# Kernel tuning notes

Hardware: AMD Instinct MI355X
Metric: run time of the kernel (lower is better)

The kernel has to match this reference:

```python
import jax, jax.numpy as jnp
import numpy as np

B, T, C, H = 2, 2048, 1024, 16
HS = C // H  # head_size = 64
EPS = 1e-5


def _layernorm(x, w, b):
    mu = jnp.mean(x, axis=-1, keepdims=True)
    var = jnp.mean(jnp.square(x - mu), axis=-1, keepdims=True)
    return (x - mu) * jax.lax.rsqrt(var + EPS) * w + b


def setup_inputs() -> dict:
    key = jax.random.key(0)
    ks = jax.random.split(key, 12)
    s_attn = 1.0 / np.sqrt(C)
    s_ff1 = 1.0 / np.sqrt(C)
    s_ff2 = 1.0 / np.sqrt(4 * C)
    return {
        "x": jax.random.normal(ks[0], (B, T, C), dtype=jnp.float32),
        "ln1_w": jnp.ones((C,), jnp.float32),
        "ln1_b": jnp.zeros((C,), jnp.float32),
        "Wq": jax.random.normal(ks[1], (H, C, HS), jnp.float32) * s_attn,
        "Wk": jax.random.normal(ks[2], (H, C, HS), jnp.float32) * s_attn,
        "Wv": jax.random.normal(ks[3], (H, C, HS), jnp.float32) * s_attn,
        "proj_w": jax.random.normal(ks[4], (C, C), jnp.float32) * s_attn,
        "proj_b": jnp.zeros((C,), jnp.float32),
        "ln2_w": jnp.ones((C,), jnp.float32),
        "ln2_b": jnp.zeros((C,), jnp.float32),
        "fc1_w": jax.random.normal(ks[5], (C, 4 * C), jnp.float32) * s_ff1,
        "fc1_b": jnp.zeros((4 * C,), jnp.float32),
        "fc2_w": jax.random.normal(ks[6], (4 * C, C), jnp.float32) * s_ff2,
        "fc2_b": jnp.zeros((C,), jnp.float32),
    }


def reference(x, ln1_w, ln1_b, Wq, Wk, Wv, proj_w, proj_b, ln2_w, ln2_b, fc1_w, fc1_b, fc2_w, fc2_b):
    Bx, Tx, Cx = x.shape
    # --- self-attention with pre-norm residual ---
    h = _layernorm(x, ln1_w, ln1_b)                       # [B,T,C]
    q = jnp.einsum("btc,hcd->bhtd", h, Wq)                 # [B,H,T,HS]
    k = jnp.einsum("btc,hcd->bhtd", h, Wk)
    v = jnp.einsum("btc,hcd->bhtd", h, Wv)
    # NOTE: original code applies NO 1/sqrt(d) scaling -- keep faithful.
    wei = jnp.einsum("bhtd,bhsd->bhts", q, k)              # [B,H,T,T]
    causal = jnp.tril(jnp.ones((Tx, Tx), dtype=bool))
    wei = jnp.where(causal, wei, -jnp.inf)
    wei = jax.nn.softmax(wei, axis=-1)
    attn = jnp.einsum("bhts,bhsd->bhtd", wei, v)           # [B,H,T,HS]
    attn = attn.transpose(0, 2, 1, 3).reshape(Bx, Tx, Cx)  # concat heads
    sa = attn @ proj_w + proj_b                            # output projection
    x = x + sa
    # --- FFN with pre-norm residual ---
    h2 = _layernorm(x, ln2_w, ln2_b)
    ff = jax.nn.relu(h2 @ fc1_w + fc1_b) @ fc2_w + fc2_b
    return x + ff
```

## Files before the change

kernel.cpp:

```cpp
#include <hip/hip_runtime.h>
#include <hip/hip_bf16.h>

#define Bn 2
#define Tn 2048
#define Cn 1024
#define Hn 16
#define HSn 64
#define Mn (Bn*Tn)
#define LN_EPS 1e-5f

typedef unsigned short u16;
typedef __attribute__((ext_vector_type(8))) short bf16x8;
typedef __attribute__((ext_vector_type(4))) float f32x4;

#define MFMA16(a,b,c) __builtin_amdgcn_mfma_f32_16x16x32_bf16(a, b, c, 0, 0, 0)
#define GLL16(g,l) __builtin_amdgcn_global_load_lds( \
    (const __attribute__((address_space(1))) void*)(g), \
    (__attribute__((address_space(3))) void*)(l), 16, 0, 0)

__device__ __forceinline__ u16 f2b(float f) {
    unsigned int u = __float_as_uint(f);
    unsigned int r = (u + 0x7FFFu + ((u >> 16) & 1u)) >> 16;
    return (u16)r;
}
__device__ __forceinline__ float b2f(unsigned u) {
    return __uint_as_float(u << 16);
}
__device__ __forceinline__ unsigned cvtpk(float lo, float hi) {
    unsigned r;
    asm("v_cvt_pk_bf16_f32 %0, %1, %2" : "=v"(r) : "v"(lo), "v"(hi));
    return r;
}

__global__ __launch_bounds__(256) void wqkv_t(
    const float* __restrict__ Wq, const float* __restrict__ Wk,
    const float* __restrict__ Wv, u16* __restrict__ Wt)
{
    int z = blockIdx.z, h = blockIdx.y, c0 = blockIdx.x * 64;
    const float* in = (z == 0 ? Wq : z == 1 ? Wk : Wv) + (size_t)h * 65536;
    __shared__ float t[64][68];
    int tid = threadIdx.x;
#pragma unroll
    for (int it = 0; it < 4; it++) {
        int r = it * 16 + (tid >> 4);
        *(float4*)&t[r][(tid & 15) * 4] =
            *(const float4*)(in + (size_t)(c0 + r) * 64 + (tid & 15) * 4);
    }
    __syncthreads();
    int d = tid >> 2, seg = tid & 3;
    union { u16 u[8]; uint4 q; } pk;
#pragma unroll
    for (int hq = 0; hq < 2; hq++) {
#pragma unroll
        for (int j = 0; j < 8; j++) pk.u[j] = f2b(t[seg * 16 + hq * 8 + j][d]);
        *(uint4*)(Wt + (size_t)(z * 1024 + h * 64 + d) * 1024 + c0 + seg * 16 + hq * 8) = pk.q;
    }
}

__global__ __launch_bounds__(256) void transpose_cvt(
    const float* __restrict__ in, u16* __restrict__ out, int R, int C)
{
    __shared__ float t[64][68];
    int r0 = blockIdx.y * 64, c0 = blockIdx.x * 64;
    int tid = threadIdx.x;
#pragma unroll
    for (int it = 0; it < 4; it++) {
        int r = it * 16 + (tid >> 4);
        *(float4*)&t[r][(tid & 15) * 4] =
            *(const float4*)(in + (size_t)(r0 + r) * C + c0 + (tid & 15) * 4);
    }
    __syncthreads();
    int c = tid >> 2, seg = tid & 3;
    union { u16 u[8]; uint4 q; } pk;
#pragma unroll
    for (int hq = 0; hq < 2; hq++) {
#pragma unroll
        for (int j = 0; j < 8; j++) pk.u[j] = f2b(t[seg * 16 + hq * 8 + j][c]);
        *(uint4*)(out + (size_t)(c0 + c) * R + r0 + seg * 16 + hq * 8) = pk.q;
    }
}

__global__ __launch_bounds__(256) void ln_bf16(
    const float* __restrict__ x, const float* __restrict__ w,
    const float* __restrict__ bvec, u16* __restrict__ out)
{
    int row  = blockIdx.x * 4 + (threadIdx.x >> 6);
    int lane = threadIdx.x & 63;
    const float* xr = x + (size_t)row * Cn;
    float4 v[4];
    float s = 0.f, sq = 0.f;
#pragma unroll
    for (int i = 0; i < 4; i++) {
        v[i] = *(const float4*)(xr + lane * 4 + i * 256);
        s  += v[i].x + v[i].y + v[i].z + v[i].w;
        sq += v[i].x * v[i].x + v[i].y * v[i].y + v[i].z * v[i].z + v[i].w * v[i].w;
    }
#pragma unroll
    for (int off = 1; off < 64; off <<= 1) {
        s  += __shfl_xor(s, off);
        sq += __shfl_xor(sq, off);
    }
    float mu   = s * (1.f / Cn);
    float var  = sq * (1.f / Cn) - mu * mu;
    float rstd = rsqrtf(var + LN_EPS);
    u16* orow = out + (size_t)row * Cn;
#pragma unroll
    for (int i = 0; i < 4; i++) {
        float4 w4 = *(const float4*)(w    + lane * 4 + i * 256);
        float4 b4 = *(const float4*)(bvec + lane * 4 + i * 256);
        union { u16 u[4]; uint2 q; } pk;
        pk.u[0] = f2b((v[i].x - mu) * rstd * w4.x + b4.x);
        pk.u[1] = f2b((v[i].y - mu) * rstd * w4.y + b4.y);
        pk.u[2] = f2b((v[i].z - mu) * rstd * w4.z + b4.z);
        pk.u[3] = f2b((v[i].w - mu) * rstd * w4.w + b4.w);
        *(uint2*)(orow + lane * 4 + i * 256) = pk.q;
    }
}

template<int OBF, int BIAS, int RELU>
__global__ __launch_bounds__(512, 2) void gemm_8ph(
    const u16* __restrict__ A, const u16* __restrict__ Bt,
    const float* __restrict__ bias, void* Cout,
    int M, int N, int K, int NT)
{
    __shared__ u16 lds[65536];
    const int tid = threadIdx.x, l = tid & 63, w = tid >> 6;
    const int wm = w >> 2, wn = w & 3;
    const int g = l >> 4, c16 = l & 15;

    const int nwg = (int)gridDim.x, cpx = nwg >> 3;
    const int bid = (int)blockIdx.x;
    const int sbid = (bid & 7) * cpx + (bid >> 3);
    const int m0 = (sbid / NT) * 256, n0 = (sbid % NT) * 256;

    const int sr = tid >> 3;
    const int ss = ((tid & 7) ^ (sr & 7)) << 3;
    const u16* Asrc = A  + (size_t)(m0 + sr) * K + ss;
    const u16* Bsrc = Bt + (size_t)(n0 + sr) * K + ss;
    const int dst0 = tid * 8;

#define ST_A8(d_, h_, kt_) do {                                              \
        GLL16(Asrc + (size_t)((h_) * 128) * K + (size_t)(kt_) * 64,          \
              &lds[(d_) * 32768 + (h_) * 8192 + dst0]);                      \
        GLL16(Asrc + (size_t)((h_) * 128 + 64) * K + (size_t)(kt_) * 64,     \
              &lds[(d_) * 32768 + (h_) * 8192 + 4096 + dst0]);               \
    } while (0)
#define ST_B8(d_, h_, kt_) do {                                              \
        GLL16(Bsrc + (size_t)((h_) * 128) * K + (size_t)(kt_) * 64,          \
              &lds[(d_) * 32768 + 16384 + (h_) * 8192 + dst0]);              \
        GLL16(Bsrc + (size_t)((h_) * 128 + 64) * K + (size_t)(kt_) * 64,     \
              &lds[(d_) * 32768 + 16384 + (h_) * 8192 + 4096 + dst0]);       \
    } while (0)
#define LDA8(d_, mi_, s_) (*(const bf16x8*)&lds[(d_) * 32768 +               \
        (wm * 128 + (mi_) * 16 + c16) * 64 +                                  \
        ((((s_) * 4 + g) ^ ((wm * 128 + (mi_) * 16 + c16) & 7)) << 3)])
#define LDB8(d_, nj_, s_) (*(const bf16x8*)&lds[(d_) * 32768 + 16384 +       \
        (wn * 64 + (nj_) * 16 + c16) * 64 +                                   \
        ((((s_) * 4 + g) ^ ((wn * 64 + (nj_) * 16 + c16) & 7)) << 3)])
#define PH_HEAD() do {                                                       \
        __builtin_amdgcn_s_barrier();                                        \
        asm volatile("s_waitcnt lgkmcnt(0)" ::: "memory");                   \
        __builtin_amdgcn_sched_barrier(0);                                   \
        __builtin_amdgcn_s_setprio(1);                                       \
    } while (0)
#define PH_MFMA(NH_) do {                                                    \
        _Pragma("unroll")                                                    \
        for (int mi = 0; mi < 8; mi++) {                                     \
            acc[mi][2*(NH_)]   = MFMA16(aF[mi], bF[0], acc[mi][2*(NH_)]);    \
            acc[mi][2*(NH_)+1] = MFMA16(aF[mi], bF[1], acc[mi][2*(NH_)+1]);  \
        }                                                                    \
    } while (0)

    f32x4 acc[8][4];
#pragma unroll
    for (int i = 0; i < 8; i++)
#pragma unroll
        for (int j = 0; j < 4; j++) acc[i][j] = (f32x4){0.f, 0.f, 0.f, 0.f};

    const int nk = K >> 6;
    ST_A8(0, 0, 0); ST_A8(0, 1, 0); ST_B8(0, 0, 0); ST_B8(0, 1, 0);
    ST_A8(1, 0, 1); ST_A8(1, 1, 1);
    asm volatile("s_waitcnt vmcnt(4)" ::: "memory");
    __builtin_amdgcn_s_barrier();

    bf16x8 aF[8], bF[2];
    for (int m = 0; m < nk; m++) {
        const int d = m & 1, dn = d ^ 1;
#pragma unroll
        for (int mi = 0; mi < 8; mi++) aF[mi] = LDA8(d, mi, 0);
        bF[0] = LDB8(d, 0, 0); bF[1] = LDB8(d, 1, 0);
        if (m + 1 < nk) ST_B8(dn, 0, m + 1);
        PH_HEAD(); PH_MFMA(0);
        __builtin_amdgcn_s_setprio(0);
        __builtin_amdgcn_s_barrier();
        bF[0] = LDB8(d, 2, 0); bF[1] = LDB8(d, 3, 0);
        if (m + 1 < nk) ST_B8(dn, 1, m + 1);
        PH_HEAD(); PH_MFMA(1);
        __builtin_amdgcn_s_setprio(0);
        __builtin_amdgcn_s_barrier();
#pragma unroll
        for (int mi = 0; mi < 8; mi++) aF[mi] = LDA8(d, mi, 1);
        bF[0] = LDB8(d, 0, 1); bF[1] = LDB8(d, 1, 1);
        PH_HEAD(); PH_MFMA(0);
        __builtin_amdgcn_s_setprio(0);
        __builtin_amdgcn_s_barrier();
        bF[0] = LDB8(d, 2, 1); bF[1] = LDB8(d, 3, 1);
        if (m + 2 < nk) { ST_A8(d, 0, m + 2); ST_A8(d, 1, m + 2); }
        PH_HEAD(); PH_MFMA(1);
        __builtin_amdgcn_s_setprio(0);
        if (m + 1 < nk) {
            if (m + 2 < nk) asm volatile("s_waitcnt vmcnt(4)" ::: "memory");
            else            asm volatile("s_waitcnt vmcnt(0)" ::: "memory");
        }
        __builtin_amdgcn_s_barrier();
    }
#undef ST_A8
#undef ST_B8
#undef LDA8
#undef LDB8
#undef PH_HEAD
#undef PH_MFMA

#pragma unroll
    for (int mi = 0; mi < 8; mi++)
#pragma unroll
        for (int nj = 0; nj < 4; nj++) {
            const int coln = n0 + wn * 64 + nj * 16 + c16;
            float bv = BIAS ? bias[coln] : 0.f;
#pragma unroll
            for (int reg = 0; reg < 4; reg++) {
                int rowm = m0 + wm * 128 + mi * 16 + 4 * g + reg;
                float v = acc[mi][nj][reg] + bv;
                if (RELU) v = fmaxf(v, 0.f);
                if (OBF) ((u16*)Cout)[(size_t)rowm * N + coln] = f2b(v);
                else     ((float*)Cout)[(size_t)rowm * N + coln] = v;
            }
        }
}

__global__ __launch_bounds__(512, 1) void gemm_qkv(
    const u16* __restrict__ A, const u16* __restrict__ Bt,
    u16* __restrict__ Cout)
{
    __shared__ u16 lds[57344];
    const int tid = threadIdx.x, l = tid & 63, w = tid >> 6;
    const int wm = w >> 1, wn = w & 1;
    const int g = l >> 4, c16 = l & 15;
    const int K = 1024, N = 3072;

    const int bid = (int)blockIdx.x;
    const int sbid = (bid & 7) * 32 + (bid >> 3);
    const int m0 = (sbid >> 4) * 256, n0 = (sbid & 15) * 192;

    const int sr = tid >> 3;
    const int ss = ((tid & 7) ^ (sr & 7)) << 3;
    const u16* Asrc = A  + (size_t)(m0 + sr) * K + ss;
    const u16* Bsrc = Bt + (size_t)(n0 + sr) * K + ss;
    const int dst0 = tid * 8;

#define ST_A(d_, h_, kt_) do {                                               \
        GLL16(Asrc + (size_t)((h_) * 128) * K + (size_t)(kt_) * 64,          \
              &lds[(d_) * 16384 + (h_) * 8192 + dst0]);                      \
        GLL16(Asrc + (size_t)((h_) * 128 + 64) * K + (size_t)(kt_) * 64,     \
              &lds[(d_) * 16384 + (h_) * 8192 + 4096 + dst0]);               \
    } while (0)
#define ST_B1(d_, seg_, kt_)                                                 \
        GLL16(Bsrc + (size_t)((seg_) * 64) * K + (size_t)(kt_) * 64,         \
              &lds[32768 + (d_) * 12288 + (seg_) * 4096 + dst0])
#define LDA(d_, mi_, s_) (*(const bf16x8*)&lds[(d_) * 16384 +                \
        (wm * 64 + (mi_) * 16 + c16) * 64 +                                   \
        ((((s_) * 4 + g) ^ ((wm * 64 + (mi_) * 16 + c16) & 7)) << 3)])
#define LDB(d_, nj_, s_) (*(const bf16x8*)&lds[32768 + (d_) * 12288 +        \
        (wn * 96 + (nj_) * 16 + c16) * 64 +                                   \
        ((((s_) * 4 + g) ^ ((wn * 96 + (nj_) * 16 + c16) & 7)) << 3)])
#define PH_HEAD() do {                                                       \
        __builtin_amdgcn_s_barrier();                                        \
        asm volatile("s_waitcnt lgkmcnt(0)" ::: "memory");                   \
        __builtin_amdgcn_sched_barrier(0);                                   \
        __builtin_amdgcn_s_setprio(1);                                       \
    } while (0)
#define PH_MFMA(NH_) do {                                                    \
        _Pragma("unroll")                                                    \
        for (int mi = 0; mi < 4; mi++) {                                     \
            acc[mi][3*(NH_)]   = MFMA16(aF[mi], bF[0], acc[mi][3*(NH_)]);    \
            acc[mi][3*(NH_)+1] = MFMA16(aF[mi], bF[1], acc[mi][3*(NH_)+1]);  \
            acc[mi][3*(NH_)+2] = MFMA16(aF[mi], bF[2], acc[mi][3*(NH_)+2]);  \
        }                                                                    \
    } while (0)

    f32x4 acc[4][6];
#pragma unroll
    for (int i = 0; i < 4; i++)
#pragma unroll
        for (int j = 0; j < 6; j++) acc[i][j] = (f32x4){0.f, 0.f, 0.f, 0.f};

    const int nk = 16;
    ST_A(0, 0, 0); ST_A(0, 1, 0);
    ST_B1(0, 0, 0); ST_B1(0, 1, 0); ST_B1(0, 2, 0);
    ST_A(1, 0, 1); ST_A(1, 1, 1);
    asm volatile("s_waitcnt vmcnt(4)" ::: "memory");
    __builtin_amdgcn_s_barrier();

    bf16x8 aF[4], bF[3];
    for (int m = 0; m < nk; m++) {
        const int d = m & 1, dn = d ^ 1;
#pragma unroll
        for (int mi = 0; mi < 4; mi++) aF[mi] = LDA(d, mi, 0);
        bF[0] = LDB(d, 0, 0); bF[1] = LDB(d, 1, 0); bF[2] = LDB(d, 2, 0);
        if (m + 1 < nk) { ST_B1(dn, 0, m + 1); ST_B1(dn, 1, m + 1); }
        PH_HEAD(); PH_MFMA(0);
        __builtin_amdgcn_s_setprio(0);
        __builtin_amdgcn_s_barrier();
        bF[0] = LDB(d, 3, 0); bF[1] = LDB(d, 4, 0); bF[2] = LDB(d, 5, 0);
        if (m + 1 < nk) ST_B1(dn, 2, m + 1);
        PH_HEAD(); PH_MFMA(1);
        __builtin_amdgcn_s_setprio(0);
        __builtin_amdgcn_s_barrier();
#pragma unroll
        for (int mi = 0; mi < 4; mi++) aF[mi] = LDA(d, mi, 1);
        bF[0] = LDB(d, 0, 1); bF[1] = LDB(d, 1, 1); bF[2] = LDB(d, 2, 1);
        PH_HEAD(); PH_MFMA(0);
        __builtin_amdgcn_s_setprio(0);
        __builtin_amdgcn_s_barrier();
        bF[0] = LDB(d, 3, 1); bF[1] = LDB(d, 4, 1); bF[2] = LDB(d, 5, 1);
        if (m + 2 < nk) { ST_A(d, 0, m + 2); ST_A(d, 1, m + 2); }
        PH_HEAD(); PH_MFMA(1);
        __builtin_amdgcn_s_setprio(0);
        if (m + 1 < nk) {
            if (m + 2 < nk) asm volatile("s_waitcnt vmcnt(4)" ::: "memory");
            else            asm volatile("s_waitcnt vmcnt(0)" ::: "memory");
        }
        __builtin_amdgcn_s_barrier();
    }
#undef ST_A
#undef ST_B1
#undef LDA
#undef LDB
#undef PH_HEAD
#undef PH_MFMA

#pragma unroll
    for (int mi = 0; mi < 4; mi++)
#pragma unroll
        for (int nj = 0; nj < 6; nj++) {
            const int coln = n0 + wn * 96 + nj * 16 + c16;
#pragma unroll
            for (int reg = 0; reg < 4; reg++) {
                int rowm = m0 + wm * 64 + mi * 16 + 4 * g + reg;
                Cout[(size_t)rowm * N + coln] = f2b(acc[mi][nj][reg]);
            }
        }
}

__global__ __launch_bounds__(512, 2) void gemm_fc2(
    const u16* __restrict__ A, const u16* __restrict__ Bt,
    u16* __restrict__ part)
{
    __shared__ u16 lds[65536];
    const int tid = threadIdx.x, l = tid & 63, w = tid >> 6;
    const int wm = w >> 2, wn = w & 3;
    const int g = l >> 4, c16 = l & 15;

    const int bid = (int)blockIdx.x;
    const int sbid = (bid & 7) * 32 + (bid >> 3);
    const int chunk = sbid >> 6, t = sbid & 63;
    const int m0 = (t >> 2) * 256, n0 = (t & 3) * 256;
    const int kB = chunk << 10;

    const int sr = tid >> 3;
    const int ss = ((tid & 7) ^ (sr & 7)) << 3;
    const u16* Asrc = A  + (size_t)(m0 + sr) * 4096 + kB + ss;
    const u16* Bsrc = Bt + (size_t)(n0 + sr) * 4096 + kB + ss;
    const int dst0 = tid * 8;

#define ST_A8(d_, h_, kt_) do {                                              \
        GLL16(Asrc + (size_t)((h_) * 128) * 4096 + (size_t)(kt_) * 64,       \
              &lds[(d_) * 32768 + (h_) * 8192 + dst0]);                      \
        GLL16(Asrc + (size_t)((h_) * 128 + 64) * 4096 + (size_t)(kt_) * 64,  \
              &lds[(d_) * 32768 + (h_) * 8192 + 4096 + dst0]);               \
    } while (0)
#define ST_B8(d_, h_, kt_) do {                                              \
        GLL16(Bsrc + (size_t)((h_) * 128) * 4096 + (size_t)(kt_) * 64,       \
              &lds[(d_) * 32768 + 16384 + (h_) * 8192 + dst0]);              \
        GLL16(Bsrc + (size_t)((h_) * 128 + 64) * 4096 + (size_t)(kt_) * 64,  \
              &lds[(d_) * 32768 + 16384 + (h_) * 8192 + 4096 + dst0]);       \
    } while (0)
#define LDA8(d_, mi_, s_) (*(const bf16x8*)&lds[(d_) * 32768 +               \
        (wm * 128 + (mi_) * 16 + c16) * 64 +                                  \
        ((((s_) * 4 + g) ^ ((wm * 128 + (mi_) * 16 + c16) & 7)) << 3)])
#define LDB8(d_, nj_, s_) (*(const bf16x8*)&lds[(d_) * 32768 + 16384 +       \
        (wn * 64 + (nj_) * 16 + c16) * 64 +                                   \
        ((((s_) * 4 + g) ^ ((wn * 64 + (nj_) * 16 + c16) & 7)) << 3)])
#define PH_HEAD() do {                                                       \
        __builtin_amdgcn_s_barrier();                                        \
        asm volatile("s_waitcnt lgkmcnt(0)" ::: "memory");                   \
        __builtin_amdgcn_sched_barrier(0);                                   \
        __builtin_amdgcn_s_setprio(1);                                       \
    } while (0)
#define PH_MFMA(NH_) do {                                                    \
        _Pragma("unroll")                                                    \
        for (int mi = 0; mi < 8; mi++) {                                     \
            acc[mi][2*(NH_)]   = MFMA16(aF[mi], bF[0], acc[mi][2*(NH_)]);    \
            acc[mi][2*(NH_)+1] = MFMA16(aF[mi], bF[1], acc[mi][2*(NH_)+1]);  \
        }                                                                    \
    } while (0)

    f32x4 acc[8][4];
#pragma unroll
    for (int i = 0; i < 8; i++)
#pragma unroll
        for (int j = 0; j < 4; j++) acc[i][j] = (f32x4){0.f, 0.f, 0.f, 0.f};

    const int nk = 16;
    ST_A8(0, 0, 0); ST_A8(0, 1, 0); ST_B8(0, 0, 0); ST_B8(0, 1, 0);
    ST_A8(1, 0, 1); ST_A8(1, 1, 1);
    asm volatile("s_waitcnt vmcnt(4)" ::: "memory");
    __builtin_amdgcn_s_barrier();

    bf16x8 aF[8], bF[2];
    for (int m = 0; m < nk; m++) {
        const int d = m & 1, dn = d ^ 1;
#pragma unroll
        for (int mi = 0; mi < 8; mi++) aF[mi] = LDA8(d, mi, 0);
        bF[0] = LDB8(d, 0, 0); bF[1] = LDB8(d, 1, 0);
        if (m + 1 < nk) ST_B8(dn, 0, m + 1);
        PH_HEAD(); PH_MFMA(0);
        __builtin_amdgcn_s_setprio(0);
        __builtin_amdgcn_s_barrier();
        bF[0] = LDB8(d, 2, 0); bF[1] = LDB8(d, 3, 0);
        if (m + 1 < nk) ST_B8(dn, 1, m + 1);
        PH_HEAD(); PH_MFMA(1);
        __builtin_amdgcn_s_setprio(0);
        __builtin_amdgcn_s_barrier();
#pragma unroll
        for (int mi = 0; mi < 8; mi++) aF[mi] = LDA8(d, mi, 1);
        bF[0] = LDB8(d, 0, 1); bF[1] = LDB8(d, 1, 1);
        PH_HEAD(); PH_MFMA(0);
        __builtin_amdgcn_s_setprio(0);
        __builtin_amdgcn_s_barrier();
        bF[0] = LDB8(d, 2, 1); bF[1] = LDB8(d, 3, 1);
        if (m + 2 < nk) { ST_A8(d, 0, m + 2); ST_A8(d, 1, m + 2); }
        PH_HEAD(); PH_MFMA(1);
        __builtin_amdgcn_s_setprio(0);
        if (m + 1 < nk) {
            if (m + 2 < nk) asm volatile("s_waitcnt vmcnt(4)" ::: "memory");
            else            asm volatile("s_waitcnt vmcnt(0)" ::: "memory");
        }
        __builtin_amdgcn_s_barrier();
    }
#undef ST_A8
#undef ST_B8
#undef LDA8
#undef LDB8
#undef PH_HEAD
#undef PH_MFMA

    u16* pp = part + (size_t)chunk * 4194304;
#pragma unroll
    for (int mi = 0; mi < 8; mi++)
#pragma unroll
        for (int nj = 0; nj < 4; nj++) {
            const int coln = n0 + wn * 64 + nj * 16 + c16;
#pragma unroll
            for (int reg = 0; reg < 4; reg++) {
                int rowm = m0 + wm * 128 + mi * 16 + 4 * g + reg;
                pp[(size_t)rowm * 1024 + coln] = f2b(acc[mi][nj][reg]);
            }
        }
}

__global__ __launch_bounds__(256) void splitk_reduce(
    const u16* __restrict__ part, const float* __restrict__ bias,
    float* __restrict__ out)
{
    size_t i = ((size_t)blockIdx.x * 256 + threadIdx.x) * 4;
    int col = (int)(i & 1023);
    float4 o  = *(float4*)(out + i);
    float4 bv = *(const float4*)(bias + col);
    float s0 = o.x + bv.x, s1 = o.y + bv.y, s2 = o.z + bv.z, s3 = o.w + bv.w;
#pragma unroll
    for (int c = 0; c < 4; c++) {
        uint2 p = *(const uint2*)(part + (size_t)c * 4194304 + i);
        s0 += b2f(p.x & 0xffffu);
        s1 += b2f(p.x >> 16);
        s2 += b2f(p.y & 0xffffu);
        s3 += b2f(p.y >> 16);
    }
    float4 r; r.x = s0; r.y = s1; r.z = s2; r.w = s3;
    *(float4*)(out + i) = r;
}

template<int OBF, int BIAS, int RES, int RELU>
__global__ __launch_bounds__(256) void gemm_n64(
    const u16* __restrict__ A, const u16* __restrict__ Bt,
    const float* __restrict__ bias, const float* res,
    void* Cout, int M, int N, int K)
{
    __shared__ u16 As[2][8192];
    __shared__ u16 Bs[2][4096];
    const int tid = threadIdx.x;
    const int l = tid & 63, w = tid >> 6;
    const int wr = w >> 1, wc = w & 1;
    const int g = l >> 4, c16 = l & 15;
    const int m0 = blockIdx.y * 128, n0 = blockIdx.x * 64;

    const u16* a_src[4];
    int a_dst[4];
#pragma unroll
    for (int i = 0; i < 4; i++) {
        int G = tid + 256 * i, r = G >> 3, sl = G & 7;
        a_src[i] = A + (size_t)(m0 + r) * K + ((sl ^ (r & 7)) << 3);
        a_dst[i] = G * 8;
    }
    const u16* b_src[2];
    int b_dst[2];
#pragma unroll
    for (int i = 0; i < 2; i++) {
        int G = tid + 256 * i, r = G >> 3, sl = G & 7;
        b_src[i] = Bt + (size_t)(n0 + r) * K + ((sl ^ (r & 7)) << 3);
        b_dst[i] = G * 8;
    }

    f32x4 acc[4][2];
#pragma unroll
    for (int i = 0; i < 4; i++)
#pragma unroll
        for (int j = 0; j < 2; j++) acc[i][j] = (f32x4){0.f, 0.f, 0.f, 0.f};

#define STAGE_N64(nb, k0) do {                                   \
        GLL16(a_src[0] + (k0), &As[nb][a_dst[0]]);               \
        GLL16(a_src[1] + (k0), &As[nb][a_dst[1]]);               \
        GLL16(a_src[2] + (k0), &As[nb][a_dst[2]]);               \
        GLL16(a_src[3] + (k0), &As[nb][a_dst[3]]);               \
        GLL16(b_src[0] + (k0), &Bs[nb][b_dst[0]]);               \
        GLL16(b_src[1] + (k0), &Bs[nb][b_dst[1]]);               \
    } while (0)

    STAGE_N64(0, 0);
    __syncthreads();

    int cur = 0;
    for (int k0 = 0; k0 < K; k0 += 64) {
        if (k0 + 64 < K) STAGE_N64(cur ^ 1, k0 + 64);
        const u16* AsC = As[cur];
        const u16* BsC = Bs[cur];
        bf16x8 af[4][2], bfr[2][2];
#pragma unroll
        for (int fi = 0; fi < 4; fi++) {
            int r = wr * 64 + fi * 16 + c16;
            af[fi][0] = *(const bf16x8*)&AsC[r * 64 + (((g    ) ^ (r & 7)) << 3)];
            af[fi][1] = *(const bf16x8*)&AsC[r * 64 + (((4 + g) ^ (r & 7)) << 3)];
        }
#pragma unroll
        for (int fj = 0; fj < 2; fj++) {
            int r = wc * 32 + fj * 16 + c16;
            bfr[fj][0] = *(const bf16x8*)&BsC[r * 64 + (((g    ) ^ (r & 7)) << 3)];
            bfr[fj][1] = *(const bf16x8*)&BsC[r * 64 + (((4 + g) ^ (r & 7)) << 3)];
        }
#pragma unroll
        for (int fi = 0; fi < 4; fi++)
#pragma unroll
            for (int fj = 0; fj < 2; fj++) {
                acc[fi][fj] = MFMA16(af[fi][0], bfr[fj][0], acc[fi][fj]);
                acc[fi][fj] = MFMA16(af[fi][1], bfr[fj][1], acc[fi][fj]);
            }
        __syncthreads();
        cur ^= 1;
    }
#undef STAGE_N64

#pragma unroll
    for (int fi = 0; fi < 4; fi++)
#pragma unroll
        for (int fj = 0; fj < 2; fj++) {
            int coln = n0 + wc * 32 + fj * 16 + c16;
            float bv = BIAS ? bias[coln] : 0.f;
#pragma unroll
            for (int reg = 0; reg < 4; reg++) {
                int rowm = m0 + wr * 64 + fi * 16 + 4 * g + reg;
                float v = acc[fi][fj][reg] + bv;
                if (RES) v += res[(size_t)rowm * N + coln];
                if (RELU) v = fmaxf(v, 0.f);
                if (OBF) ((u16*)Cout)[(size_t)rowm * N + coln] = f2b(v);
                else     ((float*)Cout)[(size_t)rowm * N + coln] = v;
            }
        }
}

__global__ __launch_bounds__(256) void v_transpose(
    const u16* __restrict__ qkv, u16* __restrict__ vT)
{
    int t0 = blockIdx.x * 64, h = blockIdx.y, b = blockIdx.z;
    __shared__ u16 t[64][72];
    int tid = threadIdx.x;
#pragma unroll
    for (int it = 0; it < 2; it++) {
        int r = it * 32 + (tid >> 3);
        int cs = (tid & 7) * 8;
        *(uint4*)&t[r][cs] =
            *(const uint4*)(qkv + (size_t)(b * 2048 + t0 + r) * 3072 + 2048 + h * 64 + cs);
    }
    __syncthreads();
    int d = tid >> 2, seg = tid & 3;
    union { u16 u[8]; uint4 q; } pk;
#pragma unroll
    for (int hq = 0; hq < 2; hq++) {
#pragma unroll
        for (int j = 0; j < 8; j++) pk.u[j] = t[seg * 16 + hq * 8 + j][d];
        *(uint4*)(vT + (size_t)((b * 16 + h) * 64 + d) * 2048 + t0 + seg * 16 + hq * 8) = pk.q;
    }
}

__global__ __launch_bounds__(512) void attn_mfma(
    const u16* __restrict__ qkv, const u16* __restrict__ vT,
    u16* __restrict__ outb)
{
    __shared__ u16 smem[24576];
    u16* KsB = smem;
    u16* VsB = smem + 8192;
    u16* PsB = smem + 16384;
    const int tid = threadIdx.x, l = tid & 63, w = tid >> 6;
    const int g = l >> 4, c16 = l & 15;
    const int qg = w & 3, kg = w >> 2;
    const int kg32 = kg * 32, kg64 = kg * 64;
    const int bh = blockIdx.y, b = bh >> 4, h = bh & 15;
    const int bx = (int)blockIdx.x;
    const int qt = (bh < 16) ? (15 - bx) : bx;
    const int r0 = qt * 128;
    const int wq0 = r0 + qg * 32;

    bf16x8 qf[2][2];
#pragma unroll
    for (int grp = 0; grp < 2; grp++) {
        const u16* qrow = qkv + (size_t)(b * 2048 + wq0 + grp * 16 + c16) * 3072 + h * 64;
        qf[grp][0] = *(const bf16x8*)(qrow + g * 8);
        qf[grp][1] = *(const bf16x8*)(qrow + 32 + g * 8);
    }

    const int kr = tid >> 3, ks = (tid & 7) ^ (kr & 7);
    const u16* kgp = qkv + (size_t)(b * 2048) * 3072 + 1024 + h * 64;
    const u16* vgp = vT + (size_t)((b * 16 + h) * 64) * 2048;

    float lrow[2] = {0.f, 0.f};
    f32x4 oacc[2][4];
#pragma unroll
    for (int grp = 0; grp < 2; grp++)
#pragma unroll
        for (int i = 0; i < 4; i++) oacc[grp][i] = (f32x4){0.f, 0.f, 0.f, 0.f};

    const int prow0 = (qg * 32 + c16) * 128;
    const int swz   = (c16 & 7) << 4;

#define STAGE_KV(nb, s0) do {                                                  \
        GLL16(kgp + (size_t)((s0) + kr) * 3072 + ks * 8, &KsB[(nb)*4096 + tid*8]); \
        GLL16(vgp + (size_t)kr * 2048 + (s0) + ks * 8, &VsB[(nb)*4096 + tid*8]);   \
    } while (0)

    STAGE_KV(0, 0);
    asm volatile("s_waitcnt vmcnt(0)" ::: "memory");
    __builtin_amdgcn_sched_barrier(0);
    __builtin_amdgcn_s_barrier();

    const int nt = 2 * qt + 2;
    int cur = 0;
    for (int kt = 0; kt < nt; kt++) {
        if (kt + 1 < nt) STAGE_KV(cur ^ 1, (kt + 1) * 64);
        if (kt > 0) {
            if (kt + 1 < nt) asm volatile("s_waitcnt vmcnt(2)" ::: "memory");
            else             asm volatile("s_waitcnt vmcnt(0)" ::: "memory");
            __builtin_amdgcn_sched_barrier(0);
            __builtin_amdgcn_s_barrier();
        }
        const u16* KsC = &KsB[cur * 4096];
        const u16* VsC = &VsB[cur * 4096];
        const int s0 = kt * 64;

        bf16x8 kf0[2], kf1[2];
#pragma unroll
        for (int fj = 0; fj < 2; fj++) {
            int r = kg32 + fj * 16 + c16;
            kf0[fj] = *(const bf16x8*)&KsC[r * 64 + ((g       ^ (r & 7)) << 3)];
            kf1[fj] = *(const bf16x8*)&KsC[r * 64 + (((4 + g) ^ (r & 7)) << 3)];
        }
#pragma unroll
        for (int grp = 0; grp < 2; grp++) {
            f32x4 sc[2];
            sc[0] = (f32x4){0.f, 0.f, 0.f, 0.f};
            sc[1] = (f32x4){0.f, 0.f, 0.f, 0.f};
#pragma unroll
            for (int fj = 0; fj < 2; fj++) {
                sc[fj] = MFMA16(kf0[fj], qf[grp][0], sc[fj]);
                sc[fj] = MFMA16(kf1[fj], qf[grp][1], sc[fj]);
            }
            const int qgl = wq0 + grp * 16 + c16;
            if (s0 + kg32 + 31 > wq0 + grp * 16) {
#pragma unroll
                for (int fj = 0; fj < 2; fj++)
#pragma unroll
                    for (int reg = 0; reg < 4; reg++)
                        if (s0 + kg32 + fj * 16 + 4 * g + reg > qgl)
                            sc[fj][reg] = -1e30f;
            }
#pragma unroll
            for (int fj = 0; fj < 2; fj++) {
                float p0 = __expf(sc[fj][0]);
                float p1 = __expf(sc[fj][1]);
                float p2 = __expf(sc[fj][2]);
                float p3 = __expf(sc[fj][3]);
                lrow[grp] += (p0 + p1) + (p2 + p3);
                uint2 pk;
                pk.x = cvtpk(p0, p1);
                pk.y = cvtpk(p2, p3);
                *(uint2*)((char*)PsB + prow0 + grp * 2048 +
                          ((kg64 + fj * 32 + 8 * g) ^ swz)) = pk;
            }
        }
        bf16x8 pa0 = *(const bf16x8*)((const char*)PsB + prow0 +
                                      ((kg64 + 16 * g) ^ swz));
        bf16x8 pa1 = *(const bf16x8*)((const char*)PsB + prow0 + 2048 +
                                      ((kg64 + 16 * g) ^ swz));
#pragma unroll
        for (int fd = 0; fd < 4; fd++) {
            int r = fd * 16 + c16;
            bf16x8 vf = *(const bf16x8*)&VsC[r * 64 + (((4 * kg + g) ^ (r & 7)) << 3)];
            oacc[0][fd] = MFMA16(pa0, vf, oacc[0][fd]);
            oacc[1][fd] = MFMA16(pa1, vf, oacc[1][fd]);
        }
        __builtin_amdgcn_s_barrier();
        cur ^= 1;
    }
#undef STAGE_KV

#pragma unroll
    for (int grp = 0; grp < 2; grp++) {
        lrow[grp] += __shfl_xor(lrow[grp], 16);
        lrow[grp] += __shfl_xor(lrow[grp], 32);
    }

    __syncthreads();
    float* scr = (float*)smem;
    const int sbase = qg * 2304 + l * 36;
    if (kg == 1) {
#pragma unroll
        for (int grp = 0; grp < 2; grp++) {
#pragma unroll
            for (int fd = 0; fd < 4; fd++)
                *(f32x4*)&scr[sbase + grp * 16 + fd * 4] = oacc[grp][fd];
            scr[sbase + 32 + grp] = lrow[grp];
        }
    }
    __syncthreads();
    if (kg == 0) {
#pragma unroll
        for (int grp = 0; grp < 2; grp++) {
#pragma unroll
            for (int fd = 0; fd < 4; fd++)
                oacc[grp][fd] += *(const f32x4*)&scr[sbase + grp * 16 + fd * 4];
            float lr = lrow[grp] + scr[sbase + 32 + grp];
#pragma unroll
            for (int reg = 0; reg < 4; reg++) {
                float ls = __shfl(lr, 4 * g + reg);
                float inv = 1.0f / ls;
                int t = wq0 + grp * 16 + 4 * g + reg;
                u16* op = outb + (size_t)(b * 2048 + t) * 1024 + h * 64;
#pragma unroll
                for (int fd = 0; fd < 4; fd++)
                    op[fd * 16 + c16] = f2b(oacc[grp][fd][reg] * inv);
            }
        }
    }
}

extern "C" void kernel_launch(void* const* d_in, const int* in_sizes, int n_in,
                              void* d_out, int out_size, void* d_ws, size_t ws_size,
                              hipStream_t stream) {
    const float* x     = (const float*)d_in[0];
    const float* ln1w  = (const float*)d_in[1];
    const float* ln1b  = (const float*)d_in[2];
    const float* Wq    = (const float*)d_in[3];
    const float* Wk    = (const float*)d_in[4];
    const float* Wv    = (const float*)d_in[5];
    const float* projw = (const float*)d_in[6];
    const float* projb = (const float*)d_in[7];
    const float* ln2w  = (const float*)d_in[8];
    const float* ln2b  = (const float*)d_in[9];
    const float* fc1w  = (const float*)d_in[10];
    const float* fc1b  = (const float*)d_in[11];
    const float* fc2w  = (const float*)d_in[12];
    const float* fc2b  = (const float*)d_in[13];
    float* out = (float*)d_out;

    u16* h_bf    = (u16*)d_ws;
    u16* qkv_bf  = h_bf    + 4194304;
    u16* vTb     = qkv_bf  + 12582912;
    u16* attn_bf = vTb     + 4194304;
    u16* ff1_bf  = attn_bf + 4194304;
    u16* WtQKV   = ff1_bf  + 16777216;
    u16* WtP     = WtQKV   + 3145728;
    u16* Wt1     = WtP     + 1048576;
    u16* Wt2     = Wt1     + 4194304;
    u16* fc2p = (u16*)d_ws;

    wqkv_t<<<dim3(16, 16, 3), 256, 0, stream>>>(Wq, Wk, Wv, WtQKV);
    transpose_cvt<<<dim3(16, 16), 256, 0, stream>>>(projw, WtP, 1024, 1024);
    transpose_cvt<<<dim3(64, 16), 256, 0, stream>>>(fc1w, Wt1, 1024, 4096);
    transpose_cvt<<<dim3(16, 64), 256, 0, stream>>>(fc2w, Wt2, 4096, 1024);

    ln_bf16<<<1024, 256, 0, stream>>>(x, ln1w, ln1b, h_bf);
    gemm_qkv<<<dim3(256), 512, 0, stream>>>(h_bf, WtQKV, qkv_bf);
    v_transpose<<<dim3(32, 16, 2), 256, 0, stream>>>(qkv_bf, vTb);
    attn_mfma<<<dim3(16, 32), 512, 0, stream>>>(qkv_bf, vTb, attn_bf);
    gemm_n64<0, 1, 1, 0><<<dim3(16, 32), 256, 0, stream>>>(
        attn_bf, WtP, projb, x, out, Mn, 1024, 1024);
    ln_bf16<<<1024, 256, 0, stream>>>(out, ln2w, ln2b, h_bf);
    gemm_8ph<1, 1, 1><<<dim3(256), 512, 0, stream>>>(
        h_bf, Wt1, fc1b, ff1_bf, Mn, 4096, 1024, 16);
    gemm_fc2<<<dim3(256), 512, 0, stream>>>(ff1_bf, Wt2, fc2p);
    splitk_reduce<<<dim3(4096), 256, 0, stream>>>(fc2p, fc2b, out);
}
```

Before: 206.1 us.

## Merge weight repack kernels and keep residual intermediate in bf16

The four weight transpose/convert launches are merged into one repack kernel that dispatches on block index, removing launch overhead. The attention projection output plus residual is now stored as bf16 instead of fp32. A new bf16-input layernorm reads it, and the split-K reduce also reads it, which cuts the memory traffic of that intermediate. The cost is lower precision in the residual stream feeding the final output.

```diff
diff --git a/kernel.cpp b/kernel.cpp
--- a/kernel.cpp
+++ b/kernel.cpp
@@ -32,42 +32,15 @@
     return r;
 }
 
-__global__ __launch_bounds__(256) void wqkv_t(
-    const float* __restrict__ Wq, const float* __restrict__ Wk,
-    const float* __restrict__ Wv, u16* __restrict__ Wt)
-{
-    int z = blockIdx.z, h = blockIdx.y, c0 = blockIdx.x * 64;
-    const float* in = (z == 0 ? Wq : z == 1 ? Wk : Wv) + (size_t)h * 65536;
-    __shared__ float t[64][68];
-    int tid = threadIdx.x;
+__device__ __forceinline__ void trans_tile(
+    const float* __restrict__ in, u16* __restrict__ out,
+    int R, int C, int r0, int c0c, float (*t)[68], int tid)
+{
 #pragma unroll
     for (int it = 0; it < 4; it++) {
         int r = it * 16 + (tid >> 4);
         *(float4*)&t[r][(tid & 15) * 4] =
-            *(const float4*)(in + (size_t)(c0 + r) * 64 + (tid & 15) * 4);
-    }
-    __syncthreads();
-    int d = tid >> 2, seg = tid & 3;
-    union { u16 u[8]; uint4 q; } pk;
-#pragma unroll
-    for (int hq = 0; hq < 2; hq++) {
-#pragma unroll
-        for (int j = 0; j < 8; j++) pk.u[j] = f2b(t[seg * 16 + hq * 8 + j][d]);
-        *(uint4*)(Wt + (size_t)(z * 1024 + h * 64 + d) * 1024 + c0 + seg * 16 + hq * 8) = pk.q;
-    }
-}
-
-__global__ __launch_bounds__(256) void transpose_cvt(
-    const float* __restrict__ in, u16* __restrict__ out, int R, int C)
-{
-    __shared__ float t[64][68];
-    int r0 = blockIdx.y * 64, c0 = blockIdx.x * 64;
-    int tid = threadIdx.x;
-#pragma unroll
-    for (int it = 0; it < 4; it++) {
-        int r = it * 16 + (tid >> 4);
-        *(float4*)&t[r][(tid & 15) * 4] =
-            *(const float4*)(in + (size_t)(r0 + r) * C + c0 + (tid & 15) * 4);
+            *(const float4*)(in + (size_t)(r0 + r) * C + c0c + (tid & 15) * 4);
     }
     __syncthreads();
     int c = tid >> 2, seg = tid & 3;
@@ -76,7 +49,33 @@
     for (int hq = 0; hq < 2; hq++) {
 #pragma unroll
         for (int j = 0; j < 8; j++) pk.u[j] = f2b(t[seg * 16 + hq * 8 + j][c]);
-        *(uint4*)(out + (size_t)(c0 + c) * R + r0 + seg * 16 + hq * 8) = pk.q;
+        *(uint4*)(out + (size_t)(c0c + c) * R + r0 + seg * 16 + hq * 8) = pk.q;
+    }
+}
+
+__global__ __launch_bounds__(256) void repack_all(
+    const float* __restrict__ Wq, const float* __restrict__ Wk,
+    const float* __restrict__ Wv, u16* __restrict__ WtQKV,
+    const float* __restrict__ projw, u16* __restrict__ WtP,
+    const float* __restrict__ fc1w, u16* __restrict__ Wt1,
+    const float* __restrict__ fc2w, u16* __restrict__ Wt2)
+{
+    __shared__ float t[64][68];
+    const int bid = (int)blockIdx.x, tid = threadIdx.x;
+    if (bid < 768) {
+        int z = bid >> 8, rem = bid & 255, h = rem >> 4, c0 = (rem & 15) * 64;
+        const float* in = (z == 0 ? Wq : z == 1 ? Wk : Wv) + (size_t)h * 65536;
+        u16* outb = WtQKV + (size_t)(z * 1024 + h * 64) * 1024;
+        trans_tile(in, outb, 1024, 64, c0, 0, t, tid);
+    } else if (bid < 1024) {
+        int idx = bid - 768, bx = idx & 15, by = idx >> 4;
+        trans_tile(projw, WtP, 1024, 1024, by * 64, bx * 64, t, tid);
+    } else if (bid < 2048) {
+        int idx = bid - 1024, bx = idx & 63, by = idx >> 6;
+        trans_tile(fc1w, Wt1, 1024, 4096, by * 64, bx * 64, t, tid);
+    } else {
+        int idx = bid - 2048, bx = idx & 15, by = idx >> 4;
+        trans_tile(fc2w, Wt2, 4096, 1024, by * 64, bx * 64, t, tid);
     }
 }
 
@@ -114,6 +113,47 @@
         pk.u[2] = f2b((v[i].z - mu) * rstd * w4.z + b4.z);
         pk.u[3] = f2b((v[i].w - mu) * rstd * w4.w + b4.w);
         *(uint2*)(orow + lane * 4 + i * 256) = pk.q;
+    }
+}
+
+__global__ __launch_bounds__(256) void ln_bf16_b(
+    const u16* __restrict__ x, const float* __restrict__ w,
+    const float* __restrict__ bvec, u16* __restrict__ out)
+{
+    int row  = blockIdx.x * 4 + (threadIdx.x >> 6);
+    int lane = threadIdx.x & 63;
+    const u16* xr = x + (size_t)row * Cn + lane * 16;
+    float v[16];
+    float s = 0.f, sq = 0.f;
+#pragma unroll
+    for (int i = 0; i < 2; i++) {
+        uint4 q = *(const uint4*)(xr + i * 8);
+        float* vv = v + i * 8;
+        vv[0] = b2f(q.x & 0xffffu); vv[1] = b2f(q.x >> 16);
+        vv[2] = b2f(q.y & 0xffffu); vv[3] = b2f(q.y >> 16);
+        vv[4] = b2f(q.z & 0xffffu); vv[5] = b2f(q.z >> 16);
+        vv[6] = b2f(q.w & 0xffffu); vv[7] = b2f(q.w >> 16);
+    }
+#pragma unroll
+    for (int j = 0; j < 16; j++) { s += v[j]; sq += v[j] * v[j]; }
+#pragma unroll
+    for (int off = 1; off < 64; off <<= 1) {
+        s  += __shfl_xor(s, off);
+        sq += __shfl_xor(sq, off);
+    }
+    float mu   = s * (1.f / Cn);
+    float var  = sq * (1.f / Cn) - mu * mu;
+    float rstd = rsqrtf(var + LN_EPS);
+    u16* orow = out + (size_t)row * Cn + lane * 16;
+#pragma unroll
+    for (int i = 0; i < 2; i++) {
+        union { u16 u[8]; uint4 q; } pk;
+#pragma unroll
+        for (int j = 0; j < 8; j++) {
+            int col = lane * 16 + i * 8 + j;
+            pk.u[j] = f2b((v[i * 8 + j] - mu) * rstd * w[col] + bvec[col]);
+        }
+        *(uint4*)(orow + i * 8) = pk.q;
     }
 }
 
@@ -470,14 +510,17 @@
 }
 
 __global__ __launch_bounds__(256) void splitk_reduce(
-    const u16* __restrict__ part, const float* __restrict__ bias,
-    float* __restrict__ out)
+    const u16* __restrict__ part, const u16* __restrict__ x1,
+    const float* __restrict__ bias, float* __restrict__ out)
 {
     size_t i = ((size_t)blockIdx.x * 256 + threadIdx.x) * 4;
     int col = (int)(i & 1023);
-    float4 o  = *(float4*)(out + i);
     float4 bv = *(const float4*)(bias + col);
-    float s0 = o.x + bv.x, s1 = o.y + bv.y, s2 = o.z + bv.z, s3 = o.w + bv.w;
+    uint2 xv = *(const uint2*)(x1 + i);
+    float s0 = b2f(xv.x & 0xffffu) + bv.x;
+    float s1 = b2f(xv.x >> 16)     + bv.y;
+    float s2 = b2f(xv.y & 0xffffu) + bv.z;
+    float s3 = b2f(xv.y >> 16)     + bv.w;
 #pragma unroll
     for (int c = 0; c < 4; c++) {
         uint2 p = *(const uint2*)(part + (size_t)c * 4194304 + i);
@@ -799,22 +842,21 @@
     u16* WtP     = WtQKV   + 3145728;
     u16* Wt1     = WtP     + 1048576;
     u16* Wt2     = Wt1     + 4194304;
+    u16* x1_bf   = Wt2     + 4194304;
     u16* fc2p = (u16*)d_ws;
 
-    wqkv_t<<<dim3(16, 16, 3), 256, 0, stream>>>(Wq, Wk, Wv, WtQKV);
-    transpose_cvt<<<dim3(16, 16), 256, 0, stream>>>(projw, WtP, 1024, 1024);
-    transpose_cvt<<<dim3(64, 16), 256, 0, stream>>>(fc1w, Wt1, 1024, 4096);
-    transpose_cvt<<<dim3(16, 64), 256, 0, stream>>>(fc2w, Wt2, 4096, 1024);
+    repack_all<<<dim3(3072), 256, 0, stream>>>(
+        Wq, Wk, Wv, WtQKV, projw, WtP, fc1w, Wt1, fc2w, Wt2);
 
     ln_bf16<<<1024, 256, 0, stream>>>(x, ln1w, ln1b, h_bf);
     gemm_qkv<<<dim3(256), 512, 0, stream>>>(h_bf, WtQKV, qkv_bf);
     v_transpose<<<dim3(32, 16, 2), 256, 0, stream>>>(qkv_bf, vTb);
     attn_mfma<<<dim3(16, 32), 512, 0, stream>>>(qkv_bf, vTb, attn_bf);
-    gemm_n64<0, 1, 1, 0><<<dim3(16, 32), 256, 0, stream>>>(
-        attn_bf, WtP, projb, x, out, Mn, 1024, 1024);
-    ln_bf16<<<1024, 256, 0, stream>>>(out, ln2w, ln2b, h_bf);
+    gemm_n64<1, 1, 1, 0><<<dim3(16, 32), 256, 0, stream>>>(
+        attn_bf, WtP, projb, x, x1_bf, Mn, 1024, 1024);
+    ln_bf16_b<<<1024, 256, 0, stream>>>(x1_bf, ln2w, ln2b, h_bf);
     gemm_8ph<1, 1, 1><<<dim3(256), 512, 0, stream>>>(
         h_bf, Wt1, fc1b, ff1_bf, Mn, 4096, 1024, 16);
     gemm_fc2<<<dim3(256), 512, 0, stream>>>(ff1_bf, Wt2, fc2p);
-    splitk_reduce<<<dim3(4096), 256, 0, stream>>>(fc2p, fc2b, out);
-}
+    splitk_reduce<<<dim3(4096), 256, 0, stream>>>(fc2p, x1_bf, fc2b, out);
+}
```

After: 199.3 us, median of 2. 1.03x faster.
